# Kernel optimization log

Hardware: AMD Instinct MI355X
Metric: run time of the kernel (lower is better)

## Reference

```python
import jax, jax.numpy as jnp
import numpy as np

N, NIN, NOUT = 8192, 512, 512


def setup_inputs() -> dict:
    key = jax.random.key(0)
    k1, k2, k3 = jax.random.split(key, 3)
    H = jax.random.normal(k1, (N, NIN), dtype=jnp.float32)
    adj_matrix = jax.random.uniform(k2, (N, N), dtype=jnp.float32)
    W = jax.random.normal(k3, (NOUT, NIN), dtype=jnp.float32) / np.sqrt(NIN)
    b = jnp.zeros((NOUT,), dtype=jnp.float32)
    return {"H": H, "adj_matrix": adj_matrix, "W": W, "b": b}


def reference(H, adj_matrix, W, b):
    n = adj_matrix.shape[0]
    # adj + I (self-loops)
    A = adj_matrix + jnp.eye(n, dtype=adj_matrix.dtype)
    # column degrees (torch.sum(dim=0))
    deg = jnp.sum(A, axis=0)
    d = deg ** -0.5
    d = jnp.where(jnp.isinf(d), 0.0, d)
    # D^-1/2 A D^-1/2 implemented as elementwise row/col rescale (same math as diag matmuls)
    A = d[:, None] * A * d[None, :]
    # message passing + linear (torch Linear: x @ W.T + b) + tanh
    Hm = A @ H  # [N, nin]
    out = jnp.tanh(Hm @ W.T + b)
    return out
```

## Files before the change

kernel.cpp:

```cpp
#include <hip/hip_runtime.h>
#include <hip/hip_bf16.h>

#define N_NODES 8192
#define N_IN 512
#define N_OUT 512

typedef __bf16 bf16;
typedef __bf16 bf16x4 __attribute__((ext_vector_type(4)));
typedef __bf16 bf16x8 __attribute__((ext_vector_type(8)));
typedef float f32x4 __attribute__((ext_vector_type(4)));

__device__ __forceinline__ void gload16(const void* g, void* l) {
  __builtin_amdgcn_global_load_lds((const __attribute__((address_space(1))) void*)g,
                                   (__attribute__((address_space(3))) void*)l, 16, 0, 0);
}

#define WAITVM(N) asm volatile("s_waitcnt vmcnt(" #N ")" ::: "memory")

__global__ __launch_bounds__(256) void k_colsum_cvt(const float* __restrict__ adj,
                                                    bf16* __restrict__ adjb,
                                                    float* __restrict__ partial) {
  const int tid  = threadIdx.x;
  const int col0 = blockIdx.x * 1024 + tid * 4;
  const int row0 = blockIdx.y * 64;
  float s0 = 0.f, s1 = 0.f, s2 = 0.f, s3 = 0.f;
#pragma unroll 4
  for (int r = 0; r < 64; ++r) {
    const float4 v = *reinterpret_cast<const float4*>(adj + (size_t)(row0 + r) * N_NODES + col0);
    s0 += v.x; s1 += v.y; s2 += v.z; s3 += v.w;
    bf16x4 o = { (bf16)v.x, (bf16)v.y, (bf16)v.z, (bf16)v.w };
    *reinterpret_cast<bf16x4*>(adjb + (size_t)(row0 + r) * N_NODES + col0) = o;
  }
  float4 ps = { s0, s1, s2, s3 };
  *reinterpret_cast<float4*>(partial + (size_t)blockIdx.y * N_NODES + col0) = ps;
}

__global__ __launch_bounds__(256) void k_dvec(const float* __restrict__ partial,
                                              float* __restrict__ dv) {
  const int j = blockIdx.x * 256 + threadIdx.x;
  float s = 1.0f;
#pragma unroll 8
  for (int p = 0; p < 128; ++p) s += partial[(size_t)p * N_NODES + j];
  dv[j] = rsqrtf(s);
}

__global__ __launch_bounds__(256) void k_hst(const float* __restrict__ H,
                                             const float* __restrict__ dv,
                                             bf16* __restrict__ Hst) {
  __shared__ float t[64][65];
  const int tid = threadIdx.x;
  const int j0 = blockIdx.x * 64;
  const int k0 = blockIdx.y * 64;
  const int rr = tid >> 4;
  const int cc = (tid & 15) * 4;
#pragma unroll
  for (int p = 0; p < 4; ++p) {
    const int r = p * 16 + rr;
    const float d = dv[j0 + r];
    float4 v = *reinterpret_cast<const float4*>(H + (size_t)(j0 + r) * N_IN + k0 + cc);
    t[r][cc + 0] = v.x * d; t[r][cc + 1] = v.y * d;
    t[r][cc + 2] = v.z * d; t[r][cc + 3] = v.w * d;
  }
  __syncthreads();
#pragma unroll
  for (int p = 0; p < 4; ++p) {
    const int kr = p * 16 + rr;
    bf16x4 o = { (bf16)t[cc + 0][kr], (bf16)t[cc + 1][kr],
                 (bf16)t[cc + 2][kr], (bf16)t[cc + 3][kr] };
    *reinterpret_cast<bf16x4*>(Hst + (size_t)(k0 + kr) * N_NODES + j0 + cc) = o;
  }
}

__global__ __launch_bounds__(256) void k_wcvt(const float* __restrict__ W, bf16* __restrict__ Wb) {
  const int i = (blockIdx.x * 256 + threadIdx.x) * 4;
  float4 v = *reinterpret_cast<const float4*>(W + i);
  bf16x4 o = { (bf16)v.x, (bf16)v.y, (bf16)v.z, (bf16)v.w };
  *reinterpret_cast<bf16x4*>(Wb + i) = o;
}

template<int KDIM, int NSPLIT>
__global__ __launch_bounds__(512, 2) void k_gemm256(
    const bf16* __restrict__ A, const bf16* __restrict__ B, float* __restrict__ P) {
  constexpr int KSEG = KDIM / NSPLIT;
  constexpr int NT = KSEG / 32;
  constexpr int NTN = 2;
  constexpr int NBLK = 32 * NTN * NSPLIT;
  __shared__ __attribute__((aligned(128))) char lds[4 * 32768];

  const int bid = blockIdx.x;
  const int logical = (bid & 7) * (NBLK / 8) + (bid >> 3);
  const int split = logical / (32 * NTN);
  const int rem = logical % (32 * NTN);
  const int bm0 = (rem >> 1) * 256;
  const int bn0 = (rem & 1) * 256;

  const int tid = threadIdx.x;
  const int lane = tid & 63;
  const int wid = tid >> 6;
  const int wr = wid >> 2;
  const int wc = wid & 3;

  const int srow = tid >> 2;
  const int scol = ((tid & 3) ^ ((srow >> 1) & 3)) << 3;
  const size_t a_src = (size_t)(bm0 + srow) * KDIM + (size_t)split * KSEG + scol;
  const size_t b_src = (size_t)(bn0 + srow) * KDIM + (size_t)split * KSEG + scol;

  const int frow = lane & 15;
  const int fk = lane >> 4;
  const int colb = (fk << 4) ^ (((frow >> 1) & 3) << 4);
  const int a_base = (wr * 128 + frow) * 64 + colb;
  const int b_base = 16384 + (wc * 64 + frow) * 64 + colb;

  f32x4 acc[8][4] = {};

  auto stage = [&](int t) {
    char* lbase = lds + (t & 3) * 32768;
    const bf16* ag = A + a_src + (size_t)t * 32;
    const bf16* bg = B + b_src + (size_t)t * 32;
    gload16(ag,                        lbase +         tid * 16);
    gload16(ag + (size_t)128 * KDIM,   lbase +  8192 + tid * 16);
    gload16(bg,                        lbase + 16384 + tid * 16);
    gload16(bg + (size_t)128 * KDIM,   lbase + 24576 + tid * 16);
  };

  auto compute = [&](int t) {
    const char* lbase = lds + (t & 3) * 32768;
    bf16x8 av[8], bv[4];
#pragma unroll
    for (int m = 0; m < 8; ++m)
      av[m] = *reinterpret_cast<const bf16x8*>(lbase + a_base + m * 1024);
#pragma unroll
    for (int n = 0; n < 4; ++n)
      bv[n] = *reinterpret_cast<const bf16x8*>(lbase + b_base + n * 1024);
    __builtin_amdgcn_s_setprio(1);
#pragma unroll
    for (int m = 0; m < 8; ++m)
#pragma unroll
      for (int n = 0; n < 4; ++n)
        acc[m][n] = __builtin_amdgcn_mfma_f32_16x16x32_bf16(av[m], bv[n], acc[m][n], 0, 0, 0);
    __builtin_amdgcn_s_setprio(0);
  };

  stage(0); stage(1); stage(2);
#pragma unroll 1
  for (int t = 0; t < NT; ++t) {
    if (t + 3 < NT) stage(t + 3);
    const int ahead = NT - 1 - t;
    if (ahead >= 3)      WAITVM(12);
    else if (ahead == 2) WAITVM(8);
    else if (ahead == 1) WAITVM(4);
    else                 WAITVM(0);
    __builtin_amdgcn_s_barrier();
    asm volatile("" ::: "memory");
    compute(t);
    asm volatile("" ::: "memory");
    __builtin_amdgcn_s_barrier();
  }

#pragma unroll
  for (int m = 0; m < 8; ++m) {
#pragma unroll
    for (int j = 0; j < 4; ++j) {
      const int grow = bm0 + wr * 128 + m * 16 + (lane >> 4) * 4 + j;
      float* prow = P + (size_t)split * ((size_t)N_NODES * N_IN) + (size_t)grow * N_IN;
#pragma unroll
      for (int n = 0; n < 4; ++n) {
        const int gcol = bn0 + wc * 64 + n * 16 + (lane & 15);
        prow[gcol] = acc[m][n][j];
      }
    }
  }
}

template<int KDIM, int NSPLIT, int EPI>
__global__ __launch_bounds__(256, 2) void k_gemm(
    const bf16* __restrict__ A, const bf16* __restrict__ B,
    const float* __restrict__ bias, float* __restrict__ outf) {
  constexpr int KSEG = KDIM / NSPLIT;
  constexpr int NT = KSEG / 64;
  constexpr int NBLK = 256 * NSPLIT;
  __shared__ __attribute__((aligned(128))) char lds[2 * 32768];

  const int bid = blockIdx.x;
  const int logical = (bid & 7) * (NBLK / 8) + (bid >> 3);
  const int split = logical & (NSPLIT - 1);
  const int tile = logical / NSPLIT;
  const int bm0 = (tile >> 2) * 128;
  const int bn0 = (tile & 3) * 128;

  const int tid = threadIdx.x;
  const int wid = tid >> 6;
  const int lane = tid & 63;
  const int wr = wid & 1, wc = wid >> 1;

  const int srow = tid >> 3;
  const int scol = ((tid & 7) ^ (srow & 7)) << 3;
  const size_t a_src = (size_t)(bm0 + srow) * KDIM + (size_t)split * KSEG + scol;
  const size_t b_src = (size_t)(bn0 + srow) * KDIM + (size_t)split * KSEG + scol;

  const int frow = lane & 15;
  const int fk = lane >> 4;
  const int swz = (lane & 7) << 4;
  const int a_row_byte = (wr * 64 + frow) * 128;
  const int b_row_byte = 16384 + (wc * 64 + frow) * 128;

  f32x4 acc[4][4] = {};

  auto stage = [&](int t) {
    char* lbase = lds + (t & 1) * 32768;
    const bf16* ag = A + a_src + (size_t)t * 64;
    const bf16* bg = B + b_src + (size_t)t * 64;
#pragma unroll
    for (int ch = 0; ch < 4; ++ch) {
      gload16(ag + (size_t)(ch * 32) * KDIM, lbase + ch * 4096 + wid * 1024);
      gload16(bg + (size_t)(ch * 32) * KDIM, lbase + 16384 + ch * 4096 + wid * 1024);
    }
  };

  auto compute = [&](int t) {
    const char* lbase = lds + (t & 1) * 32768;
#pragma unroll
    for (int kk = 0; kk < 2; ++kk) {
      const int colb = (kk * 64 + fk * 16) ^ swz;
      bf16x8 av[4], bv[4];
#pragma unroll
      for (int m = 0; m < 4; ++m)
        av[m] = *reinterpret_cast<const bf16x8*>(lbase + a_row_byte + m * 2048 + colb);
#pragma unroll
      for (int n = 0; n < 4; ++n)
        bv[n] = *reinterpret_cast<const bf16x8*>(lbase + b_row_byte + n * 2048 + colb);
#pragma unroll
      for (int m = 0; m < 4; ++m)
#pragma unroll
        for (int n = 0; n < 4; ++n)
          acc[m][n] = __builtin_amdgcn_mfma_f32_16x16x32_bf16(av[m], bv[n], acc[m][n], 0, 0, 0);
    }
  };

  stage(0);
#pragma unroll 1
  for (int t = 0; t < NT - 1; ++t) {
    stage(t + 1);
    WAITVM(8);
    __builtin_amdgcn_s_barrier();
    asm volatile("" ::: "memory");
    compute(t);
    asm volatile("" ::: "memory");
    __builtin_amdgcn_s_barrier();
  }
  WAITVM(0);
  __builtin_amdgcn_s_barrier();
  compute(NT - 1);

#pragma unroll
  for (int m = 0; m < 4; ++m) {
#pragma unroll
    for (int j = 0; j < 4; ++j) {
      const int grow = bm0 + wr * 64 + m * 16 + (lane >> 4) * 4 + j;
      float* orow = outf + (size_t)grow * N_OUT;
#pragma unroll
      for (int n = 0; n < 4; ++n) {
        const int gcol = bn0 + wc * 64 + n * 16 + (lane & 15);
        float v = acc[m][n][j] + bias[gcol];
        v = fminf(fmaxf(v, -15.f), 15.f);
        const float e = __expf(2.f * v);
        orow[gcol] = (e - 1.f) / (e + 1.f);
      }
    }
  }
}

__global__ __launch_bounds__(256) void k_red(const float* __restrict__ P,
                                             const float* __restrict__ H,
                                             const float* __restrict__ dv,
                                             bf16* __restrict__ Hm) {
  const int t = blockIdx.x * 256 + threadIdx.x;
  const int row = t >> 7;
  const int col = (t & 127) << 2;
  const size_t off = (size_t)row * N_IN + col;
  constexpr size_t S = (size_t)N_NODES * N_IN;
  const float d = dv[row];
  const float d2 = d * d;
  const float4 p0 = *reinterpret_cast<const float4*>(P + off);
  const float4 p1 = *reinterpret_cast<const float4*>(P + S + off);
  const float4 p2 = *reinterpret_cast<const float4*>(P + 2 * S + off);
  const float4 p3 = *reinterpret_cast<const float4*>(P + 3 * S + off);
  const float4 h  = *reinterpret_cast<const float4*>(H + off);
  bf16x4 o = { (bf16)(d * ((p0.x + p1.x) + (p2.x + p3.x)) + d2 * h.x),
               (bf16)(d * ((p0.y + p1.y) + (p2.y + p3.y)) + d2 * h.y),
               (bf16)(d * ((p0.z + p1.z) + (p2.z + p3.z)) + d2 * h.z),
               (bf16)(d * ((p0.w + p1.w) + (p2.w + p3.w)) + d2 * h.w) };
  *reinterpret_cast<bf16x4*>(Hm + off) = o;
}

extern "C" void kernel_launch(void* const* d_in, const int* in_sizes, int n_in,
                              void* d_out, int out_size, void* d_ws, size_t ws_size,
                              hipStream_t stream) {
  const float* H   = (const float*)d_in[0];
  const float* adj = (const float*)d_in[1];
  const float* W   = (const float*)d_in[2];
  const float* b   = (const float*)d_in[3];
  float* out = (float*)d_out;
  char* ws = (char*)d_ws;

  bf16*  adjb = (bf16*)(ws);
  bf16*  Hst  = (bf16*)(ws + 134217728);
  bf16*  Hm   = (bf16*)(ws + 142606336);
  bf16*  Wb   = (bf16*)(ws + 150994944);
  float* part = (float*)(ws + 151519232);
  float* dv   = (float*)(ws + 155713536);
  float* P    = (float*)(ws + 155746304);

  k_colsum_cvt<<<dim3(8, 128), 256, 0, stream>>>(adj, adjb, part);
  k_dvec<<<32, 256, 0, stream>>>(part, dv);
  k_hst<<<dim3(128, 8), 256, 0, stream>>>(H, dv, Hst);
  k_wcvt<<<256, 256, 0, stream>>>(W, Wb);
  k_gemm256<8192, 4><<<256, 512, 0, stream>>>(adjb, Hst, P);
  k_red<<<4096, 256, 0, stream>>>(P, H, dv, Hm);
  k_gemm<512, 1, 1><<<256, 256, 0, stream>>>(Hm, Wb, b, out);
}
```

Before: 199.2 us.

## Restructure big GEMM pipeline into split-phase interleaved prefetch and fold identity into adjb

The large adj@H GEMM now keeps two tiles in flight instead of three. Each K step is split into two halves, and the A and B prefetch global-to-LDS loads are issued between the fragment reads and the MFMA bursts, with extra barriers. The self-loop identity is added into the bf16 adjacency during the conversion pass, so the reduction kernel no longer reads H to add the d^2*H term. This saves an 8192x512 fp32 read but rounds the diagonal 1+adj to bf16, and it adds barriers per iteration.

```diff
diff --git a/kernel.cpp b/kernel.cpp
--- a/kernel.cpp
+++ b/kernel.cpp
@@ -16,6 +16,8 @@
 }
 
 #define WAITVM(N) asm volatile("s_waitcnt vmcnt(" #N ")" ::: "memory")
+#define BAR() do { asm volatile("" ::: "memory"); __builtin_amdgcn_s_barrier(); \
+                   asm volatile("" ::: "memory"); } while (0)
 
 __global__ __launch_bounds__(256) void k_colsum_cvt(const float* __restrict__ adj,
                                                     bf16* __restrict__ adjb,
@@ -26,8 +28,10 @@
   float s0 = 0.f, s1 = 0.f, s2 = 0.f, s3 = 0.f;
 #pragma unroll 4
   for (int r = 0; r < 64; ++r) {
-    const float4 v = *reinterpret_cast<const float4*>(adj + (size_t)(row0 + r) * N_NODES + col0);
+    float4 v = *reinterpret_cast<const float4*>(adj + (size_t)(row0 + r) * N_NODES + col0);
     s0 += v.x; s1 += v.y; s2 += v.z; s3 += v.w;
+    const int dq = row0 + r - col0;
+    if ((unsigned)dq < 4u) reinterpret_cast<float*>(&v)[dq] += 1.0f;
     bf16x4 o = { (bf16)v.x, (bf16)v.y, (bf16)v.z, (bf16)v.w };
     *reinterpret_cast<bf16x4*>(adjb + (size_t)(row0 + r) * N_NODES + col0) = o;
   }
@@ -113,48 +117,65 @@
 
   f32x4 acc[8][4] = {};
 
-  auto stage = [&](int t) {
-    char* lbase = lds + (t & 3) * 32768;
+  auto stage_full = [&](int t) {
+    char* sb = lds + (t & 3) * 32768;
     const bf16* ag = A + a_src + (size_t)t * 32;
     const bf16* bg = B + b_src + (size_t)t * 32;
-    gload16(ag,                        lbase +         tid * 16);
-    gload16(ag + (size_t)128 * KDIM,   lbase +  8192 + tid * 16);
-    gload16(bg,                        lbase + 16384 + tid * 16);
-    gload16(bg + (size_t)128 * KDIM,   lbase + 24576 + tid * 16);
+    gload16(ag,                      sb +         tid * 16);
+    gload16(ag + (size_t)128 * KDIM, sb +  8192 + tid * 16);
+    gload16(bg,                      sb + 16384 + tid * 16);
+    gload16(bg + (size_t)128 * KDIM, sb + 24576 + tid * 16);
   };
 
-  auto compute = [&](int t) {
+  stage_full(0); stage_full(1);
+  WAITVM(4);
+  BAR();
+
+#pragma unroll 1
+  for (int t = 0; t < NT; ++t) {
     const char* lbase = lds + (t & 3) * 32768;
+    char* sbase = lds + ((t + 2) & 3) * 32768;
+    const bf16* ag = A + a_src + (size_t)(t + 2) * 32;
+    const bf16* bg = B + b_src + (size_t)(t + 2) * 32;
+    const bool pf = (t + 2 < NT);
+
     bf16x8 av[8], bv[4];
 #pragma unroll
-    for (int m = 0; m < 8; ++m)
+    for (int m = 0; m < 4; ++m)
       av[m] = *reinterpret_cast<const bf16x8*>(lbase + a_base + m * 1024);
 #pragma unroll
     for (int n = 0; n < 4; ++n)
       bv[n] = *reinterpret_cast<const bf16x8*>(lbase + b_base + n * 1024);
+    if (pf) {
+      gload16(ag,                      sbase +        tid * 16);
+      gload16(ag + (size_t)128 * KDIM, sbase + 8192 + tid * 16);
+    }
+    BAR();
     __builtin_amdgcn_s_setprio(1);
 #pragma unroll
-    for (int m = 0; m < 8; ++m)
+    for (int m = 0; m < 4; ++m)
 #pragma unroll
       for (int n = 0; n < 4; ++n)
         acc[m][n] = __builtin_amdgcn_mfma_f32_16x16x32_bf16(av[m], bv[n], acc[m][n], 0, 0, 0);
     __builtin_amdgcn_s_setprio(0);
-  };
-
-  stage(0); stage(1); stage(2);
-#pragma unroll 1
-  for (int t = 0; t < NT; ++t) {
-    if (t + 3 < NT) stage(t + 3);
-    const int ahead = NT - 1 - t;
-    if (ahead >= 3)      WAITVM(12);
-    else if (ahead == 2) WAITVM(8);
-    else if (ahead == 1) WAITVM(4);
-    else                 WAITVM(0);
-    __builtin_amdgcn_s_barrier();
-    asm volatile("" ::: "memory");
-    compute(t);
-    asm volatile("" ::: "memory");
-    __builtin_amdgcn_s_barrier();
+    BAR();
+#pragma unroll
+    for (int m = 4; m < 8; ++m)
+      av[m] = *reinterpret_cast<const bf16x8*>(lbase + a_base + m * 1024);
+    if (pf) {
+      gload16(bg,                      sbase + 16384 + tid * 16);
+      gload16(bg + (size_t)128 * KDIM, sbase + 24576 + tid * 16);
+    }
+    BAR();
+    __builtin_amdgcn_s_setprio(1);
+#pragma unroll
+    for (int m = 4; m < 8; ++m)
+#pragma unroll
+      for (int n = 0; n < 4; ++n)
+        acc[m][n] = __builtin_amdgcn_mfma_f32_16x16x32_bf16(av[m], bv[n], acc[m][n], 0, 0, 0);
+    __builtin_amdgcn_s_setprio(0);
+    if (pf) WAITVM(4); else WAITVM(0);
+    BAR();
   }
 
 #pragma unroll
@@ -172,21 +193,18 @@
   }
 }
 
-template<int KDIM, int NSPLIT, int EPI>
+template<int KDIM>
 __global__ __launch_bounds__(256, 2) void k_gemm(
     const bf16* __restrict__ A, const bf16* __restrict__ B,
     const float* __restrict__ bias, float* __restrict__ outf) {
-  constexpr int KSEG = KDIM / NSPLIT;
-  constexpr int NT = KSEG / 64;
-  constexpr int NBLK = 256 * NSPLIT;
+  constexpr int NT = KDIM / 64;
+  constexpr int NBLK = 256;
   __shared__ __attribute__((aligned(128))) char lds[2 * 32768];
 
   const int bid = blockIdx.x;
   const int logical = (bid & 7) * (NBLK / 8) + (bid >> 3);
-  const int split = logical & (NSPLIT - 1);
-  const int tile = logical / NSPLIT;
-  const int bm0 = (tile >> 2) * 128;
-  const int bn0 = (tile & 3) * 128;
+  const int bm0 = (logical >> 2) * 128;
+  const int bn0 = (logical & 3) * 128;
 
   const int tid = threadIdx.x;
   const int wid = tid >> 6;
@@ -195,8 +213,8 @@
 
   const int srow = tid >> 3;
   const int scol = ((tid & 7) ^ (srow & 7)) << 3;
-  const size_t a_src = (size_t)(bm0 + srow) * KDIM + (size_t)split * KSEG + scol;
-  const size_t b_src = (size_t)(bn0 + srow) * KDIM + (size_t)split * KSEG + scol;
+  const size_t a_src = (size_t)(bm0 + srow) * KDIM + scol;
+  const size_t b_src = (size_t)(bn0 + srow) * KDIM + scol;
 
   const int frow = lane & 15;
   const int fk = lane >> 4;
@@ -242,14 +260,12 @@
   for (int t = 0; t < NT - 1; ++t) {
     stage(t + 1);
     WAITVM(8);
-    __builtin_amdgcn_s_barrier();
-    asm volatile("" ::: "memory");
+    BAR();
     compute(t);
-    asm volatile("" ::: "memory");
-    __builtin_amdgcn_s_barrier();
+    BAR();
   }
   WAITVM(0);
-  __builtin_amdgcn_s_barrier();
+  BAR();
   compute(NT - 1);
 
 #pragma unroll
@@ -271,7 +287,6 @@
 }
 
 __global__ __launch_bounds__(256) void k_red(const float* __restrict__ P,
-                                             const float* __restrict__ H,
                                              const float* __restrict__ dv,
                                              bf16* __restrict__ Hm) {
   const int t = blockIdx.x * 256 + threadIdx.x;
@@ -280,16 +295,14 @@
   const size_t off = (size_t)row * N_IN + col;
   constexpr size_t S = (size_t)N_NODES * N_IN;
   const float d = dv[row];
-  const float d2 = d * d;
   const float4 p0 = *reinterpret_cast<const float4*>(P + off);
   const float4 p1 = *reinterpret_cast<const float4*>(P + S + off);
   const float4 p2 = *reinterpret_cast<const float4*>(P + 2 * S + off);
   const float4 p3 = *reinterpret_cast<const float4*>(P + 3 * S + off);
-  const float4 h  = *reinterpret_cast<const float4*>(H + off);
-  bf16x4 o = { (bf16)(d * ((p0.x + p1.x) + (p2.x + p3.x)) + d2 * h.x),
-               (bf16)(d * ((p0.y + p1.y) + (p2.y + p3.y)) + d2 * h.y),
-               (bf16)(d * ((p0.z + p1.z) + (p2.z + p3.z)) + d2 * h.z),
-               (bf16)(d * ((p0.w + p1.w) + (p2.w + p3.w)) + d2 * h.w) };
+  bf16x4 o = { (bf16)(d * ((p0.x + p1.x) + (p2.x + p3.x))),
+               (bf16)(d * ((p0.y + p1.y) + (p2.y + p3.y))),
+               (bf16)(d * ((p0.z + p1.z) + (p2.z + p3.z))),
+               (bf16)(d * ((p0.w + p1.w) + (p2.w + p3.w))) };
   *reinterpret_cast<bf16x4*>(Hm + off) = o;
 }
 
@@ -316,6 +329,6 @@
   k_hst<<<dim3(128, 8), 256, 0, stream>>>(H, dv, Hst);
   k_wcvt<<<256, 256, 0, stream>>>(W, Wb);
   k_gemm256<8192, 4><<<256, 512, 0, stream>>>(adjb, Hst, P);
-  k_red<<<4096, 256, 0, stream>>>(P, H, dv, Hm);
-  k_gemm<512, 1, 1><<<256, 256, 0, stream>>>(Hm, Wb, b, out);
-}
+  k_red<<<4096, 256, 0, stream>>>(P, dv, Hm);
+  k_gemm<512><<<256, 256, 0, stream>>>(Hm, Wb, b, out);
+}
```

Result: slower. 212.2 us (+6.5%).
